# Optimization experiments

Measured on AMD Instinct MI355X. Metric: run time of the kernel, lower is better.

Reference implementation:

```python
import jax, jax.numpy as jnp
import numpy as np

N = 50000        # num nodes
E = 1_000_000    # num edges
F_IN = 256       # input feature dim
UNITS = 128      # hidden units
NUM_CLASSES = 40 # output classes
EPS = 1e-3       # Keras BatchNormalization default epsilon


def setup_inputs() -> dict:
    key = jax.random.key(0)
    ks = jax.random.split(key, 32)
    inp = {
        "x": jax.random.normal(ks[0], (N, F_IN), jnp.float32),
        "edge_index": jax.random.randint(ks[1], (2, E), 0, N, jnp.int32),
        "edge_weight": jax.random.uniform(ks[2], (E,), jnp.float32),
    }
    dims = [(F_IN, UNITS), (UNITS, UNITS), (UNITS, NUM_CLASSES)]
    ki = 3
    for li, (fi, fo) in enumerate(dims, 1):
        inp[f"w_gcn{li}"] = jax.random.normal(ks[ki], (fi, fo), jnp.float32) / np.sqrt(fi).astype(np.float32); ki += 1
        inp[f"w_self{li}"] = jax.random.normal(ks[ki], (fi, fo), jnp.float32) / np.sqrt(fi).astype(np.float32); ki += 1
        inp[f"b{li}"] = jnp.zeros((fo,), jnp.float32)
        inp[f"gamma{li}"] = 1.0 + 0.1 * jax.random.normal(ks[ki], (fo,), jnp.float32); ki += 1
        inp[f"beta{li}"] = 0.1 * jax.random.normal(ks[ki], (fo,), jnp.float32); ki += 1
        inp[f"mean{li}"] = 0.1 * jax.random.normal(ks[ki], (fo,), jnp.float32); ki += 1
        inp[f"var{li}"] = jnp.ones((fo,), jnp.float32)
    return inp


def _gcn_bs(h, src, dst, norm_w, w_gcn, w_self, b, gamma, beta, mean, var, act):
    # GCN aggregation: transform then gather->weight->scatter-sum
    hw = h @ w_gcn                                   # [N, out]
    msg = hw[src] * norm_w[:, None]                  # [E, out]
    agg = jax.ops.segment_sum(msg, dst, num_segments=N)
    out = agg + h @ w_self + b                       # self-loop dense + bias
    # BatchNorm (inference: moving stats)
    out = (out - mean) * jax.lax.rsqrt(var + EPS) * gamma + beta
    return act(out) if act is not None else out


def reference(x, edge_index, edge_weight,
              w_gcn1, w_self1, b1, gamma1, beta1, mean1, var1,
              w_gcn2, w_self2, b2, gamma2, beta2, mean2, var2,
              w_gcn3, w_self3, b3, gamma3, beta3, mean3, var3):
    src, dst = edge_index[0], edge_index[1]
    # symmetric GCN normalization (renorm=False: no added self loops)
    deg = jax.ops.segment_sum(edge_weight, dst, num_segments=N)
    dinv = jnp.where(deg > 0, jax.lax.rsqrt(jnp.where(deg > 0, deg, 1.0)), 0.0)
    norm_w = dinv[src] * edge_weight * dinv[dst]
    # inference: DropEdge and Dropout are identity
    h = _gcn_bs(x, src, dst, norm_w, w_gcn1, w_self1, b1, gamma1, beta1, mean1, var1, jax.nn.relu)
    h = _gcn_bs(h, src, dst, norm_w, w_gcn2, w_self2, b2, gamma2, beta2, mean2, var2, jax.nn.relu)
    h = _gcn_bs(h, src, dst, norm_w, w_gcn3, w_self3, b3, gamma3, beta3, mean3, var3, None)
    return h
```

## Files before the change

kernel.cpp:

```cpp
#include <hip/hip_runtime.h>
#include <hip/hip_bf16.h>

#define NN 50000
#define EE 1000000
static constexpr float EPSV = 1e-3f;
static constexpr float FIXSCALE = 16777216.f;

typedef __attribute__((ext_vector_type(8))) short short8;
typedef __attribute__((ext_vector_type(4))) float fx4;

__device__ inline float blo(unsigned u) { return __uint_as_float(u << 16); }
__device__ inline float bhi(unsigned u) { return __uint_as_float(u & 0xffff0000u); }
__device__ inline unsigned short f2b(float f) {
    __hip_bfloat16 h = __float2bfloat16(f);
    return *(unsigned short*)&h;
}
__device__ inline unsigned pack2(float a, float b) {
    return (unsigned)f2b(a) | ((unsigned)f2b(b) << 16);
}

__device__ inline void gload_lds16(const unsigned short* g, unsigned short* ldsbase) {
    __builtin_amdgcn_global_load_lds(
        (const __attribute__((address_space(1))) unsigned int*)(const void*)g,
        (__attribute__((address_space(3))) unsigned int*)(void*)ldsbase, 16, 0, 0);
}


#define ZB 196
#define WB1 256
#define WB2 128
#define WB3 64

__global__ void setup_kernel(unsigned long long* __restrict__ cnt64p,
                             const float* __restrict__ wg1, const float* __restrict__ ws1,
                             unsigned short* __restrict__ Wt1,
                             const float* __restrict__ wg2, const float* __restrict__ ws2,
                             unsigned short* __restrict__ Wt2,
                             const float* __restrict__ wg3, const float* __restrict__ ws3,
                             unsigned short* __restrict__ Wt3) {
    int b = blockIdx.x;
    int t = threadIdx.x;
    if (b < ZB) {
        int i = b * 256 + t;
        if (i < NN) cnt64p[(size_t)i << 3] = 0ull;
    } else if (b < ZB + WB1) {
        int idx = (b - ZB) * 256 + t;
        int n = idx >> 8, k = idx & 255;
        float v = (n < 128) ? wg1[(size_t)k * 128 + n]
                            : ws1[(size_t)k * 128 + (n - 128)];
        Wt1[idx] = f2b(v);
    } else if (b < ZB + WB1 + WB2) {
        int idx = (b - ZB - WB1) * 256 + t;
        int n = idx >> 7, k = idx & 127;
        float v = (n < 128) ? wg2[(size_t)k * 128 + n]
                            : ws2[(size_t)k * 128 + (n - 128)];
        Wt2[idx] = f2b(v);
    } else {
        int idx = (b - ZB - WB1 - WB2) * 256 + t;
        int n = idx >> 7, k = idx & 127;
        float v = 0.f;
        if (n < 40) v = wg3[(size_t)k * 40 + n];
        else if (n < 80) v = ws3[(size_t)k * 40 + (n - 40)];
        Wt3[idx] = f2b(v);
    }
}


#define CBH 1954
#define XBH 6250

__global__ void preA_kernel(const int* __restrict__ ei, const float* __restrict__ ew,
                            unsigned long long* __restrict__ cnt64p, unsigned* __restrict__ rank,
                            const float4* __restrict__ x, uint2* __restrict__ xb) {
    int b = blockIdx.x;
    int t = threadIdx.x;
    if (b < CBH) {
        int e = b * 256 + t;
        if (e < 500000) {
            int d = ei[EE + e];
            unsigned fx = __float2uint_rn(ew[e] * FIXSCALE);
            unsigned long long old =
                atomicAdd(&cnt64p[(size_t)d << 3], 0x100000000ull | (unsigned long long)fx);
            rank[e] = (unsigned)(old >> 32);
        }
    } else {
        int i = (b - CBH) * 256 + t;
        float4 v = x[i];
        xb[i] = make_uint2(pack2(v.x, v.y), pack2(v.z, v.w));
    }
}

__global__ void preB_kernel(const int* __restrict__ ei, const float* __restrict__ ew,
                            unsigned long long* __restrict__ cnt64p, unsigned* __restrict__ rank,
                            const float4* __restrict__ x, uint2* __restrict__ xb) {
    int b = blockIdx.x;
    int t = threadIdx.x;
    if (b < CBH) {
        int e = 500000 + b * 256 + t;
        if (e < EE) {
            int d = ei[EE + e];
            unsigned fx = __float2uint_rn(ew[e] * FIXSCALE);
            unsigned long long old =
                atomicAdd(&cnt64p[(size_t)d << 3], 0x100000000ull | (unsigned long long)fx);
            rank[e] = (unsigned)(old >> 32);
        }
    } else {
        int i = 1600000 + (b - CBH) * 256 + t;
        float4 v = x[i];
        xb[i] = make_uint2(pack2(v.x, v.y), pack2(v.z, v.w));
    }
}


__global__ __launch_bounds__(1024) void dinvsum_kernel(const unsigned long long* __restrict__ cnt64p,
                                                       float* __restrict__ dinv,
                                                       int* __restrict__ bsum) {
    __shared__ int s[1024];
    const int t = threadIdx.x;
    int idx = blockIdx.x * 1024 + t;
    unsigned long long cv = 0ull;
    if (idx < NN) cv = cnt64p[(size_t)idx << 3];
    float deg = (float)(unsigned)cv * (1.f / FIXSCALE);
    if (idx < NN) dinv[idx] = (deg > 0.f) ? rsqrtf(deg) : 0.f;
    s[t] = (int)(unsigned)(cv >> 32);
    __syncthreads();
#pragma unroll
    for (int off = 512; off > 0; off >>= 1) {
        if (t < off) s[t] += s[t + off];
        __syncthreads();
    }
    if (t == 0) bsum[blockIdx.x] = s[0];
}

__global__ __launch_bounds__(64) void scanB_kernel(const int* __restrict__ bsum,
                                                   int* __restrict__ bpre, int nb) {
    int t = threadIdx.x;
    int v = (t < nb) ? bsum[t] : 0;
    int own = v;
#pragma unroll
    for (int off = 1; off < 64; off <<= 1) {
        int u = __shfl_up(v, off);
        if (t >= off) v += u;
    }
    if (t < nb) bpre[t] = v - own;
}

__global__ __launch_bounds__(1024) void scanC_kernel(const unsigned long long* __restrict__ cnt64p,
                                                     const int* __restrict__ bpre,
                                                     int* __restrict__ rowstart) {
    __shared__ int s[1024];
    const int t = threadIdx.x;
    int idx = blockIdx.x * 1024 + t;
    int v = (idx < NN) ? (int)(unsigned)(cnt64p[(size_t)idx << 3] >> 32) : 0;
    s[t] = v;
    __syncthreads();
#pragma unroll
    for (int off = 1; off < 1024; off <<= 1) {
        int u = (t >= off) ? s[t - off] : 0;
        __syncthreads();
        s[t] += u;
        __syncthreads();
    }
    if (idx < NN) rowstart[idx] = s[t] - v + bpre[blockIdx.x];
    if (idx == 0) rowstart[NN] = EE;
}

__global__ void fill_kernel(const int* __restrict__ ei, const float* __restrict__ ew,
                            const float* __restrict__ dinv, const int* __restrict__ rowstart,
                            const unsigned* __restrict__ rank, unsigned* __restrict__ eprec4) {
    int e = blockIdx.x * blockDim.x + threadIdx.x;
    if (e >= EE) return;
    int s = ei[e], d = ei[EE + e];
    int idx = rowstart[d] + (int)rank[e];
    float w = dinv[s] * ew[e] * dinv[d];
    eprec4[idx] = ((unsigned)s << 16) | (unsigned)f2b(w);
}


__global__ __launch_bounds__(256, 6) void gemm_mfma(const unsigned short* __restrict__ Ab,
                                                    const unsigned short* __restrict__ Wt,
                                                    const float* __restrict__ bias,
                                                    unsigned short* __restrict__ Cg,
                                                    unsigned short* __restrict__ Cs,
                                                    int M, int K, int Fo) {
    __shared__ unsigned short sA[64 * 64];
    __shared__ unsigned short sB[128 * 64];

    const int t = threadIdx.x;
    const int lane = t & 63;
    const int wave = t >> 6;
    const int l15 = lane & 15, quad = lane >> 4;
    const int row0 = blockIdx.x * 64;
    const int colbase = blockIdx.y * 128;

    fx4 acc[4][2];
#pragma unroll
    for (int r = 0; r < 4; ++r)
#pragma unroll
        for (int c = 0; c < 2; ++c) acc[r][c] = (fx4){0.f, 0.f, 0.f, 0.f};

    for (int kc = 0; kc < K; kc += 64) {
#pragma unroll
        for (int j = 0; j < 6; ++j) {
            int o = wave * 6 + j;
            int ak = kc + (o & 1) * 32 + quad * 8;
            if (o < 8) {
                int ar = row0 + (o >> 1) * 16 + l15;
                if (ar >= M) ar = M - 1;
                gload_lds16(Ab + (size_t)ar * K + ak, sA + o * 512);
            } else {
                int bo = o - 8;
                int br = colbase + (bo >> 1) * 16 + l15;
                gload_lds16(Wt + (size_t)br * K + ak, sB + bo * 512);
            }
        }
        __syncthreads();

#pragma unroll
        for (int kh = 0; kh < 2; ++kh) {
            short8 a[4], b[2];
#pragma unroll
            for (int r = 0; r < 4; ++r)
                a[r] = *reinterpret_cast<const short8*>(&sA[(r * 2 + kh) * 512 + lane * 8]);
#pragma unroll
            for (int c = 0; c < 2; ++c)
                b[c] = *reinterpret_cast<const short8*>(&sB[((wave * 2 + c) * 2 + kh) * 512 + lane * 8]);
#pragma unroll
            for (int r = 0; r < 4; ++r)
#pragma unroll
                for (int c = 0; c < 2; ++c)
                    acc[r][c] = __builtin_amdgcn_mfma_f32_16x16x32_bf16(a[r], b[c], acc[r][c], 0, 0, 0);
        }
        __syncthreads();
    }

#pragma unroll
    for (int r = 0; r < 4; ++r) {
#pragma unroll
        for (int reg = 0; reg < 4; ++reg) {
            int row = row0 + r * 16 + quad * 4 + reg;
            if (row >= M) continue;
#pragma unroll
            for (int c = 0; c < 2; ++c) {
                int f = colbase + wave * 32 + c * 16 + l15;
                if (f >= 2 * Fo) continue;
                bool isG = (f < Fo);
                int col = isG ? f : f - Fo;
                float badd = isG ? 0.f : bias[col];
                unsigned short* basep = isG ? Cg : Cs;
                basep[(size_t)row * Fo + col] = f2b(acc[r][c][reg] + badd);
            }
        }
    }
}


template <bool RELU>
__global__ __launch_bounds__(256) void agg128_kernel(
    const int* __restrict__ rowstart, const unsigned* __restrict__ eprec4,
    const unsigned* __restrict__ hw, const unsigned* __restrict__ selfC,
    const float* __restrict__ g, const float* __restrict__ be,
    const float* __restrict__ mu, const float* __restrict__ va,
    unsigned* __restrict__ out) {
    int wave = threadIdx.x >> 6;
    int lane = threadIdx.x & 63;
    int n = blockIdx.x * 4 + wave;
    if (n >= NN) return;
    unsigned scp = selfC[n * 64 + lane];
    float acc0 = blo(scp), acc1 = bhi(scp);
    int beg = rowstart[n], end = rowstart[n + 1];
    int i = beg;

    if (i + 8 <= end) {
        unsigned e[8];
        {
            int ifl = __builtin_amdgcn_readfirstlane(i);
#pragma unroll
            for (int k = 0; k < 8; ++k) e[k] = eprec4[ifl + k];
        }
        for (; i + 16 <= end; i += 8) {
            unsigned v[8];
#pragma unroll
            for (int k = 0; k < 8; ++k) v[k] = hw[(e[k] >> 16) * 64u + lane];
            unsigned en[8];
            {
                int ifl = __builtin_amdgcn_readfirstlane(i + 8);
#pragma unroll
                for (int k = 0; k < 8; ++k) en[k] = eprec4[ifl + k];
            }
#pragma unroll
            for (int k = 0; k < 8; ++k) {
                float w = blo(e[k]);
                acc0 += blo(v[k]) * w;
                acc1 += bhi(v[k]) * w;
            }
#pragma unroll
            for (int k = 0; k < 8; ++k) e[k] = en[k];
        }
        unsigned v[8];
#pragma unroll
        for (int k = 0; k < 8; ++k) v[k] = hw[(e[k] >> 16) * 64u + lane];
#pragma unroll
        for (int k = 0; k < 8; ++k) {
            float w = blo(e[k]);
            acc0 += blo(v[k]) * w;
            acc1 += bhi(v[k]) * w;
        }
        i += 8;
    }
    for (; i + 4 <= end; i += 4) {
        unsigned e0 = eprec4[i], e1 = eprec4[i + 1], e2 = eprec4[i + 2], e3 = eprec4[i + 3];
        unsigned v0 = hw[(e0 >> 16) * 64u + lane];
        unsigned v1 = hw[(e1 >> 16) * 64u + lane];
        unsigned v2 = hw[(e2 >> 16) * 64u + lane];
        unsigned v3 = hw[(e3 >> 16) * 64u + lane];
        float w0 = blo(e0), w1 = blo(e1), w2 = blo(e2), w3 = blo(e3);
        acc0 += blo(v0) * w0; acc1 += bhi(v0) * w0;
        acc0 += blo(v1) * w1; acc1 += bhi(v1) * w1;
        acc0 += blo(v2) * w2; acc1 += bhi(v2) * w2;
        acc0 += blo(v3) * w3; acc1 += bhi(v3) * w3;
    }
    for (; i < end; ++i) {
        unsigned e = eprec4[i];
        unsigned v = hw[(e >> 16) * 64u + lane];
        float w = blo(e);
        acc0 += blo(v) * w; acc1 += bhi(v) * w;
    }
    float2 m2 = reinterpret_cast<const float2*>(mu)[lane];
    float2 v2f = reinterpret_cast<const float2*>(va)[lane];
    float2 g2 = reinterpret_cast<const float2*>(g)[lane];
    float2 b2 = reinterpret_cast<const float2*>(be)[lane];
    float r0 = (acc0 - m2.x) * rsqrtf(v2f.x + EPSV) * g2.x + b2.x;
    float r1 = (acc1 - m2.y) * rsqrtf(v2f.y + EPSV) * g2.y + b2.y;
    if (RELU) {
        r0 = fmaxf(r0, 0.f);
        r1 = fmaxf(r1, 0.f);
    }
    out[n * 64 + lane] = pack2(r0, r1);
}


__global__ __launch_bounds__(256) void agg40_kernel(
    const int* __restrict__ rowstart, const unsigned* __restrict__ eprec4,
    const unsigned* __restrict__ hw, const unsigned* __restrict__ selfC,
    const float* __restrict__ g, const float* __restrict__ be,
    const float* __restrict__ mu, const float* __restrict__ va,
    float* __restrict__ out) {
    int wave = threadIdx.x >> 6;
    int lane = threadIdx.x & 63;
    int n = blockIdx.x * 4 + wave;
    if (n >= NN) return;
    int grp = lane / 20;
    int fl = lane - grp * 20;
    float acc0 = 0.f, acc1 = 0.f;
    int beg = rowstart[n], end = rowstart[n + 1];
    if (grp < 3) {
        int i = beg + grp;
        for (; i + 9 < end; i += 12) {
            unsigned e0 = eprec4[i], e1 = eprec4[i + 3], e2 = eprec4[i + 6], e3 = eprec4[i + 9];
            unsigned v0 = hw[(e0 >> 16) * 20u + fl];
            unsigned v1 = hw[(e1 >> 16) * 20u + fl];
            unsigned v2 = hw[(e2 >> 16) * 20u + fl];
            unsigned v3 = hw[(e3 >> 16) * 20u + fl];
            float w0 = blo(e0), w1 = blo(e1), w2 = blo(e2), w3 = blo(e3);
            acc0 += blo(v0) * w0; acc1 += bhi(v0) * w0;
            acc0 += blo(v1) * w1; acc1 += bhi(v1) * w1;
            acc0 += blo(v2) * w2; acc1 += bhi(v2) * w2;
            acc0 += blo(v3) * w3; acc1 += bhi(v3) * w3;
        }
        for (; i < end; i += 3) {
            unsigned e = eprec4[i];
            unsigned v = hw[(e >> 16) * 20u + fl];
            float w = blo(e);
            acc0 += blo(v) * w;
            acc1 += bhi(v) * w;
        }
    }
    acc0 += __shfl(acc0, lane + 20) + __shfl(acc0, lane + 40);
    acc1 += __shfl(acc1, lane + 20) + __shfl(acc1, lane + 40);
    if (lane < 20) {
        int f0 = lane * 2;
        unsigned scp = selfC[n * 20 + lane];
        acc0 += blo(scp);
        acc1 += bhi(scp);
        float2 m2 = reinterpret_cast<const float2*>(mu)[lane];
        float2 v2f = reinterpret_cast<const float2*>(va)[lane];
        float2 g2 = reinterpret_cast<const float2*>(g)[lane];
        float2 b2 = reinterpret_cast<const float2*>(be)[lane];
        float r0 = (acc0 - m2.x) * rsqrtf(v2f.x + EPSV) * g2.x + b2.x;
        float r1 = (acc1 - m2.y) * rsqrtf(v2f.y + EPSV) * g2.y + b2.y;
        *reinterpret_cast<float2*>(&out[(size_t)n * 40 + f0]) = make_float2(r0, r1);
    }
}


extern "C" void kernel_launch(void* const* d_in, const int* in_sizes, int n_in,
                              void* d_out, int out_size, void* d_ws, size_t ws_size,
                              hipStream_t stream) {
    const float* x = (const float*)d_in[0];
    const int* ei = (const int*)d_in[1];
    const float* ew = (const float*)d_in[2];

    const float* wg[3]  = {(const float*)d_in[3],  (const float*)d_in[10], (const float*)d_in[17]};
    const float* wsf[3] = {(const float*)d_in[4],  (const float*)d_in[11], (const float*)d_in[18]};
    const float* bs[3]  = {(const float*)d_in[5],  (const float*)d_in[12], (const float*)d_in[19]};
    const float* gm[3]  = {(const float*)d_in[6],  (const float*)d_in[13], (const float*)d_in[20]};
    const float* bt[3]  = {(const float*)d_in[7],  (const float*)d_in[14], (const float*)d_in[21]};
    const float* mu[3]  = {(const float*)d_in[8],  (const float*)d_in[15], (const float*)d_in[22]};
    const float* vr[3]  = {(const float*)d_in[9],  (const float*)d_in[16], (const float*)d_in[23]};

    float* W = (float*)d_ws;
    float* dinv     = W + 100096;
    unsigned* rank  = (unsigned*)(W + 150144);
    int*   bsum     = (int*)(W + 1150144);
    int*   bpre     = (int*)(W + 1150208);
    int*   rowstart = (int*)(W + 1150272);
    unsigned* eprec4 = (unsigned*)(W + 1200384);
    unsigned short* Wt1 = (unsigned short*)(W + 2200384);
    unsigned short* Wt2 = (unsigned short*)(W + 2233152);
    unsigned short* Wt3 = (unsigned short*)(W + 2249536);
    unsigned short* xb  = (unsigned short*)(W + 2257728);
    unsigned short* bufH = (unsigned short*)(W + 2257728);
    unsigned short* bufHW = (unsigned short*)(W + 8657728);
    unsigned short* bufSb = (unsigned short*)(W + 11857728);
    unsigned long long* cnt64p = (unsigned long long*)(W + 11857728);

    const int B = 256;
    const int SB = 49;

    setup_kernel<<<ZB + WB1 + WB2 + WB3, B, 0, stream>>>(
        cnt64p, wg[0], wsf[0], Wt1, wg[1], wsf[1], Wt2, wg[2], wsf[2], Wt3);

    preA_kernel<<<CBH + XBH, B, 0, stream>>>(ei, ew, cnt64p, rank, (const float4*)x, (uint2*)xb);
    preB_kernel<<<CBH + XBH, B, 0, stream>>>(ei, ew, cnt64p, rank, (const float4*)x, (uint2*)xb);

    dinvsum_kernel<<<SB, 1024, 0, stream>>>(cnt64p, dinv, bsum);
    scanB_kernel<<<1, 64, 0, stream>>>(bsum, bpre, SB);
    scanC_kernel<<<SB, 1024, 0, stream>>>(cnt64p, bpre, rowstart);
    fill_kernel<<<(EE + B - 1) / B, B, 0, stream>>>(ei, ew, dinv, rowstart, rank, eprec4);

    const int aggGrid = (NN + 3) / 4;
    dim3 g2((NN + 63) / 64, 2), g1((NN + 63) / 64, 1);

    gemm_mfma<<<g2, B, 0, stream>>>(xb, Wt1, bs[0], bufHW, bufSb, NN, 256, 128);
    agg128_kernel<true><<<aggGrid, B, 0, stream>>>(rowstart, eprec4, (const unsigned*)bufHW,
                                                   (const unsigned*)bufSb, gm[0], bt[0], mu[0], vr[0],
                                                   (unsigned*)bufH);

    gemm_mfma<<<g2, B, 0, stream>>>(bufH, Wt2, bs[1], bufHW, bufSb, NN, 128, 128);
    agg128_kernel<true><<<aggGrid, B, 0, stream>>>(rowstart, eprec4, (const unsigned*)bufHW,
                                                   (const unsigned*)bufSb, gm[1], bt[1], mu[1], vr[1],
                                                   (unsigned*)bufH);

    gemm_mfma<<<g1, B, 0, stream>>>(bufH, Wt3, bs[2], bufHW, bufSb, NN, 128, 40);
    agg40_kernel<<<aggGrid, B, 0, stream>>>(rowstart, eprec4, (const unsigned*)bufHW,
                                            (const unsigned*)bufSb, gm[2], bt[2], mu[2], vr[2],
                                            (float*)d_out);
}
```

Measured before the change: 383.4 us.

## Fuse x bf16 conversion into first GEMM and deepen aggregation gather batching

The separate pass that converts x to bf16 is removed. The first GEMM now reads fp32 x directly, packs it to bf16 and writes it into LDS, and the two pre-pass launches become one atomic-count kernel. This avoids writing and re-reading a bf16 copy of x. The cost is that the x path of that GEMM loses the async global-to-LDS load, and because gemm blocks have two column tiles each x row is converted twice. The 128-wide aggregation also prefetches 16 edges at a time instead of 8 for more memory-level parallelism, at the cost of more registers, and launch_bounds min-blocks was dropped.

```diff
diff --git a/kernel.cpp b/kernel.cpp
--- a/kernel.cpp
+++ b/kernel.cpp
@@ -66,48 +66,17 @@
 }
 
 
-#define CBH 1954
-#define XBH 6250
-
-__global__ void preA_kernel(const int* __restrict__ ei, const float* __restrict__ ew,
-                            unsigned long long* __restrict__ cnt64p, unsigned* __restrict__ rank,
-                            const float4* __restrict__ x, uint2* __restrict__ xb) {
-    int b = blockIdx.x;
-    int t = threadIdx.x;
-    if (b < CBH) {
-        int e = b * 256 + t;
-        if (e < 500000) {
-            int d = ei[EE + e];
-            unsigned fx = __float2uint_rn(ew[e] * FIXSCALE);
-            unsigned long long old =
-                atomicAdd(&cnt64p[(size_t)d << 3], 0x100000000ull | (unsigned long long)fx);
-            rank[e] = (unsigned)(old >> 32);
-        }
-    } else {
-        int i = (b - CBH) * 256 + t;
-        float4 v = x[i];
-        xb[i] = make_uint2(pack2(v.x, v.y), pack2(v.z, v.w));
-    }
-}
-
-__global__ void preB_kernel(const int* __restrict__ ei, const float* __restrict__ ew,
-                            unsigned long long* __restrict__ cnt64p, unsigned* __restrict__ rank,
-                            const float4* __restrict__ x, uint2* __restrict__ xb) {
-    int b = blockIdx.x;
-    int t = threadIdx.x;
-    if (b < CBH) {
-        int e = 500000 + b * 256 + t;
-        if (e < EE) {
-            int d = ei[EE + e];
-            unsigned fx = __float2uint_rn(ew[e] * FIXSCALE);
-            unsigned long long old =
-                atomicAdd(&cnt64p[(size_t)d << 3], 0x100000000ull | (unsigned long long)fx);
-            rank[e] = (unsigned)(old >> 32);
-        }
-    } else {
-        int i = 1600000 + (b - CBH) * 256 + t;
-        float4 v = x[i];
-        xb[i] = make_uint2(pack2(v.x, v.y), pack2(v.z, v.w));
+#define CB 3907
+
+__global__ void pre_kernel(const int* __restrict__ ei, const float* __restrict__ ew,
+                           unsigned long long* __restrict__ cnt64p, unsigned* __restrict__ rank) {
+    int e = blockIdx.x * 256 + threadIdx.x;
+    if (e < EE) {
+        int d = ei[EE + e];
+        unsigned fx = __float2uint_rn(ew[e] * FIXSCALE);
+        unsigned long long old =
+            atomicAdd(&cnt64p[(size_t)d << 3], 0x100000000ull | (unsigned long long)fx);
+        rank[e] = (unsigned)(old >> 32);
     }
 }
 
@@ -177,12 +146,13 @@
 }
 
 
-__global__ __launch_bounds__(256, 6) void gemm_mfma(const unsigned short* __restrict__ Ab,
-                                                    const unsigned short* __restrict__ Wt,
-                                                    const float* __restrict__ bias,
-                                                    unsigned short* __restrict__ Cg,
-                                                    unsigned short* __restrict__ Cs,
-                                                    int M, int K, int Fo) {
+template <bool AF32>
+__global__ __launch_bounds__(256) void gemm_mfma(const void* __restrict__ Av,
+                                                 const unsigned short* __restrict__ Wt,
+                                                 const float* __restrict__ bias,
+                                                 unsigned short* __restrict__ Cg,
+                                                 unsigned short* __restrict__ Cs,
+                                                 int M, int K, int Fo) {
     __shared__ unsigned short sA[64 * 64];
     __shared__ unsigned short sB[128 * 64];
 
@@ -207,7 +177,19 @@
             if (o < 8) {
                 int ar = row0 + (o >> 1) * 16 + l15;
                 if (ar >= M) ar = M - 1;
-                gload_lds16(Ab + (size_t)ar * K + ak, sA + o * 512);
+                if constexpr (AF32) {
+                    const float* Af = (const float*)Av;
+                    const float4* p = (const float4*)(Af + (size_t)ar * K + ak);
+                    float4 v0 = p[0], v1 = p[1];
+                    uint4 u;
+                    u.x = pack2(v0.x, v0.y);
+                    u.y = pack2(v0.z, v0.w);
+                    u.z = pack2(v1.x, v1.y);
+                    u.w = pack2(v1.z, v1.w);
+                    *reinterpret_cast<uint4*>(sA + o * 512 + lane * 8) = u;
+                } else {
+                    gload_lds16((const unsigned short*)Av + (size_t)ar * K + ak, sA + o * 512);
+                }
             } else {
                 int bo = o - 8;
                 int br = colbase + (bo >> 1) * 16 + l15;
@@ -271,42 +253,42 @@
     int beg = rowstart[n], end = rowstart[n + 1];
     int i = beg;
 
-    if (i + 8 <= end) {
-        unsigned e[8];
+    if (i + 16 <= end) {
+        unsigned e[16];
         {
             int ifl = __builtin_amdgcn_readfirstlane(i);
 #pragma unroll
-            for (int k = 0; k < 8; ++k) e[k] = eprec4[ifl + k];
-        }
-        for (; i + 16 <= end; i += 8) {
-            unsigned v[8];
-#pragma unroll
-            for (int k = 0; k < 8; ++k) v[k] = hw[(e[k] >> 16) * 64u + lane];
-            unsigned en[8];
+            for (int k = 0; k < 16; ++k) e[k] = eprec4[ifl + k];
+        }
+        for (; i + 32 <= end; i += 16) {
+            unsigned v[16];
+#pragma unroll
+            for (int k = 0; k < 16; ++k) v[k] = hw[(e[k] >> 16) * 64u + lane];
+            unsigned en[16];
             {
-                int ifl = __builtin_amdgcn_readfirstlane(i + 8);
-#pragma unroll
-                for (int k = 0; k < 8; ++k) en[k] = eprec4[ifl + k];
+                int ifl = __builtin_amdgcn_readfirstlane(i + 16);
+#pragma unroll
+                for (int k = 0; k < 16; ++k) en[k] = eprec4[ifl + k];
             }
 #pragma unroll
-            for (int k = 0; k < 8; ++k) {
+            for (int k = 0; k < 16; ++k) {
                 float w = blo(e[k]);
                 acc0 += blo(v[k]) * w;
                 acc1 += bhi(v[k]) * w;
             }
 #pragma unroll
-            for (int k = 0; k < 8; ++k) e[k] = en[k];
-        }
-        unsigned v[8];
-#pragma unroll
-        for (int k = 0; k < 8; ++k) v[k] = hw[(e[k] >> 16) * 64u + lane];
-#pragma unroll
-        for (int k = 0; k < 8; ++k) {
+            for (int k = 0; k < 16; ++k) e[k] = en[k];
+        }
+        unsigned v[16];
+#pragma unroll
+        for (int k = 0; k < 16; ++k) v[k] = hw[(e[k] >> 16) * 64u + lane];
+#pragma unroll
+        for (int k = 0; k < 16; ++k) {
             float w = blo(e[k]);
             acc0 += blo(v[k]) * w;
             acc1 += bhi(v[k]) * w;
         }
-        i += 8;
+        i += 16;
     }
     for (; i + 4 <= end; i += 4) {
         unsigned e0 = eprec4[i], e1 = eprec4[i + 1], e2 = eprec4[i + 2], e3 = eprec4[i + 3];
@@ -419,7 +401,6 @@
     unsigned short* Wt1 = (unsigned short*)(W + 2200384);
     unsigned short* Wt2 = (unsigned short*)(W + 2233152);
     unsigned short* Wt3 = (unsigned short*)(W + 2249536);
-    unsigned short* xb  = (unsigned short*)(W + 2257728);
     unsigned short* bufH = (unsigned short*)(W + 2257728);
     unsigned short* bufHW = (unsigned short*)(W + 8657728);
     unsigned short* bufSb = (unsigned short*)(W + 11857728);
@@ -431,8 +412,7 @@
     setup_kernel<<<ZB + WB1 + WB2 + WB3, B, 0, stream>>>(
         cnt64p, wg[0], wsf[0], Wt1, wg[1], wsf[1], Wt2, wg[2], wsf[2], Wt3);
 
-    preA_kernel<<<CBH + XBH, B, 0, stream>>>(ei, ew, cnt64p, rank, (const float4*)x, (uint2*)xb);
-    preB_kernel<<<CBH + XBH, B, 0, stream>>>(ei, ew, cnt64p, rank, (const float4*)x, (uint2*)xb);
+    pre_kernel<<<CB, B, 0, stream>>>(ei, ew, cnt64p, rank);
 
     dinvsum_kernel<<<SB, 1024, 0, stream>>>(cnt64p, dinv, bsum);
     scanB_kernel<<<1, 64, 0, stream>>>(bsum, bpre, SB);
@@ -442,17 +422,17 @@
     const int aggGrid = (NN + 3) / 4;
     dim3 g2((NN + 63) / 64, 2), g1((NN + 63) / 64, 1);
 
-    gemm_mfma<<<g2, B, 0, stream>>>(xb, Wt1, bs[0], bufHW, bufSb, NN, 256, 128);
+    gemm_mfma<true><<<g2, B, 0, stream>>>(x, Wt1, bs[0], bufHW, bufSb, NN, 256, 128);
     agg128_kernel<true><<<aggGrid, B, 0, stream>>>(rowstart, eprec4, (const unsigned*)bufHW,
                                                    (const unsigned*)bufSb, gm[0], bt[0], mu[0], vr[0],
                                                    (unsigned*)bufH);
 
-    gemm_mfma<<<g2, B, 0, stream>>>(bufH, Wt2, bs[1], bufHW, bufSb, NN, 128, 128);
+    gemm_mfma<false><<<g2, B, 0, stream>>>(bufH, Wt2, bs[1], bufHW, bufSb, NN, 128, 128);
     agg128_kernel<true><<<aggGrid, B, 0, stream>>>(rowstart, eprec4, (const unsigned*)bufHW,
                                                    (const unsigned*)bufSb, gm[1], bt[1], mu[1], vr[1],
                                                    (unsigned*)bufH);
 
-    gemm_mfma<<<g1, B, 0, stream>>>(bufH, Wt3, bs[2], bufHW, bufSb, NN, 128, 40);
+    gemm_mfma<false><<<g1, B, 0, stream>>>(bufH, Wt3, bs[2], bufHW, bufSb, NN, 128, 40);
     agg40_kernel<<<aggGrid, B, 0, stream>>>(rowstart, eprec4, (const unsigned*)bufHW,
                                             (const unsigned*)bufSb, gm[2], bt[2], mu[2], vr[2],
                                             (float*)d_out);
```

Result: slower. 392.1 us (+2.3%).
